# Optimization experiments

Hardware: AMD Instinct MI355X
Metric: run time of the kernel (lower is better)

Reference implementation:

```python
import jax, jax.numpy as jnp
import numpy as np
from itertools import combinations

SEQ_LEN = 8
FEAT = 2048
SET_SIZE = 2
DOUT = 1152
WAY = 5
SHOT = 5
NQ = 500
MAX_LEN = int(SEQ_LEN * 1.5)
LN_EPS = 1e-5

TUPLES = np.array(list(combinations(range(SEQ_LEN), SET_SIZE)), dtype=np.int32)  # [T, SET_SIZE]
T_LEN = TUPLES.shape[0]  # C(8,2) = 28

def _positional_encoding(d_model, max_len):
    pos = np.arange(max_len, dtype=np.float32)[:, None]
    div = np.exp(np.arange(0, d_model, 2, dtype=np.float32) * (-np.log(10000.0) / d_model))
    pe = np.zeros((max_len, d_model), dtype=np.float32)
    pe[:, 0::2] = np.sin(pos * div)
    pe[:, 1::2] = np.cos(pos * div)
    return jnp.asarray(pe)

PE = _positional_encoding(FEAT, MAX_LEN)  # dropout is identity in eval mode

def _layernorm(x, gamma, beta):
    mu = jnp.mean(x, axis=-1, keepdims=True)
    var = jnp.var(x, axis=-1, keepdims=True)
    return (x - mu) * jax.lax.rsqrt(var + LN_EPS) * gamma + beta

def setup_inputs() -> dict:
    key = jax.random.key(0)
    ks = jax.random.split(key, 8)
    din = FEAT * SET_SIZE
    sc = 1.0 / np.sqrt(din)
    return {
        "support_set": jax.random.normal(ks[0], (WAY * SHOT, SEQ_LEN, FEAT), jnp.float32),
        "support_labels": jnp.repeat(jnp.arange(WAY, dtype=jnp.int32), SHOT),  # sorted, balanced episode
        "queries": jax.random.normal(ks[1], (NQ, SEQ_LEN, FEAT), jnp.float32),
        "k_w": jax.random.normal(ks[2], (din, DOUT), jnp.float32) * sc,
        "k_b": jnp.zeros((DOUT,), jnp.float32),
        "v_w": jax.random.normal(ks[3], (din, DOUT), jnp.float32) * sc,
        "v_b": jnp.zeros((DOUT,), jnp.float32),
        "ln_k_gamma": jnp.ones((DOUT,), jnp.float32),
        "ln_k_beta": jnp.zeros((DOUT,), jnp.float32),
        "global_temperature": jnp.asarray(1.0, jnp.float32),
        "temperature_weight": jnp.ones((1,), jnp.float32),
    }

def reference(support_set, support_labels, queries, k_w, k_b, v_w, v_b,
              ln_k_gamma, ln_k_beta, global_temperature, temperature_weight):
    n_q = queries.shape[0]
    # positional encoding (dropout is eval-mode identity)
    s = support_set + PE[:SEQ_LEN]
    q = queries + PE[:SEQ_LEN]
    # gather frame tuples: [n, T, SET_SIZE, FEAT] -> [n, T, SET_SIZE*FEAT]
    s_t = s[:, TUPLES, :].reshape(WAY * SHOT, T_LEN, SET_SIZE * FEAT)
    q_t = q[:, TUPLES, :].reshape(n_q, T_LEN, SET_SIZE * FEAT)
    # K / V projections; LayerNorm only on K (as in the module)
    s_ks = _layernorm(s_t @ k_w + k_b, ln_k_gamma, ln_k_beta)
    q_ks = _layernorm(q_t @ k_w + k_b, ln_k_gamma, ln_k_beta)
    s_vs = s_t @ v_w + v_b
    q_vs = q_t @ v_w + v_b
    # labels are sorted & balanced -> per-class slices are a reshape
    class_k = s_ks.reshape(WAY, SHOT, T_LEN, DOUT)
    class_v = s_vs.reshape(WAY, SHOT, T_LEN, DOUT)
    # scores[c,q,t,k,u] = <q_ks[q,t], class_k[c,k,u]> / sqrt(DOUT)
    scores = jnp.einsum('qtd,ckud->cqtku', q_ks, class_k) / np.sqrt(DOUT)
    # softmax jointly over (support-clip k, support-tuple u) per query tuple t
    attn = jax.nn.softmax(scores.reshape(WAY, n_q, T_LEN, SHOT * T_LEN), axis=-1)
    attn = attn.reshape(WAY, n_q, T_LEN, SHOT, T_LEN)
    # prototype = sum over support clips of attn @ class_v
    proto = jnp.einsum('cqtku,ckud->cqtd', attn, class_v)  # [WAY, NQ, T, DOUT]
    diff = q_vs[None] - proto
    dist = jnp.sum(diff * diff, axis=(-2, -1)) / T_LEN  # [WAY, NQ]
    logits = (-dist * global_temperature * temperature_weight[0]).T  # [NQ, WAY]
    return logits
```

## Files before the change

### kernel.cpp

```cpp
#include <hip/hip_runtime.h>

typedef __bf16 bf16;
typedef __attribute__((ext_vector_type(8))) __bf16 bf16x8;
typedef __attribute__((ext_vector_type(4))) float f32x4;

#define AS1 __attribute__((address_space(1)))
#define AS3 __attribute__((address_space(3)))

__device__ __constant__ int c_T0[28] = {0,0,0,0,0,0,0,1,1,1,1,1,1,2,2,2,2,2,3,3,3,3,4,4,4,5,5,6};
__device__ __constant__ int c_T1[28] = {1,2,3,4,5,6,7,2,3,4,5,6,7,3,4,5,6,7,4,5,6,7,5,6,7,6,7,7};

__global__ __launch_bounds__(256) void fill_pack(
    const float* __restrict__ queries, const float* __restrict__ support,
    const float* __restrict__ kw, const float* __restrict__ vw,
    bf16* __restrict__ X, bf16* __restrict__ Wp)
{
    __shared__ float t[32][33];
    const int tid = threadIdx.x;
    if (blockIdx.x < 4224) {
        const int f = blockIdx.x;
        bf16* row = X + (long)f * 2048;
        const int d0 = tid << 3;
        if (f >= 4200) {
            bf16x8 z;
            #pragma unroll
            for (int i = 0; i < 8; ++i) z[i] = (bf16)0.f;
            *(bf16x8*)(row + d0) = z;
            return;
        }
        const float* src = (f < 4000) ? (queries + (long)f * 2048)
                                      : (support + (long)(f - 4000) * 2048);
        const int s = f & 7;
        bf16x8 o;
        #pragma unroll
        for (int i = 0; i < 8; ++i) {
            int d = d0 + i;
            float dv = __expf((float)(d >> 1) * -0.008994473019508f);
            float ang = (float)s * dv;
            float pe = (d & 1) ? __cosf(ang) : __sinf(ang);
            o[i] = (bf16)(src[d] + pe);
        }
        *(bf16x8*)(row + d0) = o;
    } else {
        const int b = blockIdx.x - 4224;
        const int k0 = (b & 63) << 5, n0g = (b >> 6) << 5;
        const int tx = tid & 31, ty = tid >> 5;
        const int j = n0g / 1152, nc = n0g % 1152;
        const float* src = ((j < 2) ? kw : vw) + (long)(((j & 1) << 11) + k0) * 1152 + nc;
        #pragma unroll
        for (int i = 0; i < 4; ++i)
            t[ty + (i << 3)][tx] = src[(long)(ty + (i << 3)) * 1152 + tx];
        __syncthreads();
        #pragma unroll
        for (int i = 0; i < 4; ++i)
            Wp[(long)(n0g + ty + (i << 3)) * 2048 + k0 + tx] = (bf16)t[tx][ty + (i << 3)];
    }
}

template <typename OutT>
__global__ __launch_bounds__(256) void gemm_bt(
    const bf16* __restrict__ A, long lda, const bf16* __restrict__ B, long ldb,
    OutT* __restrict__ C, int N, int K, float scale, int tiles_n)
{
    __shared__ __align__(16) bf16 lA[128 * 32];
    __shared__ __align__(16) bf16 lB[128 * 32];
    const int tid = threadIdx.x;
    const int wid = tid >> 6, lane = tid & 63;
    const int wm = (wid >> 1) << 6, wn = (wid & 1) << 6;
    const int quad = lane >> 4, l16 = lane & 15;
    const int tm = blockIdx.x / tiles_n, tn = blockIdx.x % tiles_n;
    const int m0 = tm << 7, n0 = tn << 7;
    const bf16* Abase = A + (long)m0 * lda;

    f32x4 acc[4][4];
    #pragma unroll
    for (int i = 0; i < 4; ++i)
        #pragma unroll
        for (int j = 0; j < 4; ++j)
            #pragma unroll
            for (int r = 0; r < 4; ++r) acc[i][j][r] = 0.f;

    const int srow = lane >> 2, scol = (lane & 3) << 3;
    for (int kk = 0; kk < K; kk += 32) {
        __syncthreads();
        #pragma unroll
        for (int p = 0; p < 2; ++p) {
            const int rbase = (wid << 5) + (p << 4);
            const bf16* ga = Abase + (long)(rbase + srow) * lda + kk + scol;
            const bf16* gb = B + (long)(n0 + rbase + srow) * ldb + kk + scol;
            __builtin_amdgcn_global_load_lds((const AS1 unsigned int*)ga,
                                             (AS3 unsigned int*)(lA + rbase * 32), 16, 0, 0);
            __builtin_amdgcn_global_load_lds((const AS1 unsigned int*)gb,
                                             (AS3 unsigned int*)(lB + rbase * 32), 16, 0, 0);
        }
        __builtin_amdgcn_s_waitcnt(0);
        __syncthreads();
        bf16x8 af[4], bfr[4];
        #pragma unroll
        for (int i = 0; i < 4; ++i)
            af[i] = *(const bf16x8*)(lA + (wm + (i << 4) + l16) * 32 + (quad << 3));
        #pragma unroll
        for (int j = 0; j < 4; ++j)
            bfr[j] = *(const bf16x8*)(lB + (wn + (j << 4) + l16) * 32 + (quad << 3));
        #pragma unroll
        for (int i = 0; i < 4; ++i)
            #pragma unroll
            for (int j = 0; j < 4; ++j)
                acc[i][j] = __builtin_amdgcn_mfma_f32_16x16x32_bf16(af[i], bfr[j], acc[i][j], 0, 0, 0);
    }
    #pragma unroll
    for (int i = 0; i < 4; ++i) {
        const int row = m0 + wm + (i << 4) + (quad << 2);
        #pragma unroll
        for (int j = 0; j < 4; ++j) {
            const int col = n0 + wn + (j << 4) + l16;
            OutT* cp = C + (long)row * N + col;
            #pragma unroll
            for (int r = 0; r < 4; ++r) cp[(long)r * N] = (OutT)(acc[i][j][r] * scale);
        }
    }
}

__global__ __launch_bounds__(256) void gemm_frames(
    const bf16* __restrict__ H, const bf16* __restrict__ Bk,
    const bf16* __restrict__ svs, bf16* __restrict__ FG, bf16* __restrict__ Gb)
{
    __shared__ __align__(16) bf16 lA[128 * 32];
    __shared__ __align__(16) bf16 lB[128 * 32];
    const int tid = threadIdx.x;
    const int wid = tid >> 6, lane = tid & 63;
    const int wm = (wid >> 1) << 6, wn = (wid & 1) << 6;
    const int quad = lane >> 4, l16 = lane & 15;
    const bool gram = (int)blockIdx.x >= 792;
    int seg = 4, tm, tn;
    const bf16* Abase;
    long la;
    const bf16* B;
    if (!gram) {
        seg = blockIdx.x / 198;
        int r = blockIdx.x % 198;
        tm = r / 6; tn = r % 6;
        Abase = H + seg * 1152 + (long)(tm << 7) * 4608;
        la = 4608;
        B = (seg < 2) ? Bk : svs;
    } else {
        int r = blockIdx.x - 792;
        tm = r / 6; tn = r % 6;
        Abase = svs + (long)(tm << 7) * 1152;
        la = 1152;
        B = svs;
    }
    const int n0 = tn << 7;

    f32x4 acc[4][4];
    #pragma unroll
    for (int i = 0; i < 4; ++i)
        #pragma unroll
        for (int j = 0; j < 4; ++j)
            #pragma unroll
            for (int r = 0; r < 4; ++r) acc[i][j][r] = 0.f;

    const int srow = lane >> 2, scol = (lane & 3) << 3;
    for (int kk = 0; kk < 1152; kk += 32) {
        __syncthreads();
        #pragma unroll
        for (int p = 0; p < 2; ++p) {
            const int rbase = (wid << 5) + (p << 4);
            const bf16* ga = Abase + (long)(rbase + srow) * la + kk + scol;
            const bf16* gb = B + (long)(n0 + rbase + srow) * 1152 + kk + scol;
            __builtin_amdgcn_global_load_lds((const AS1 unsigned int*)ga,
                                             (AS3 unsigned int*)(lA + rbase * 32), 16, 0, 0);
            __builtin_amdgcn_global_load_lds((const AS1 unsigned int*)gb,
                                             (AS3 unsigned int*)(lB + rbase * 32), 16, 0, 0);
        }
        __builtin_amdgcn_s_waitcnt(0);
        __syncthreads();
        bf16x8 af[4], bfr[4];
        #pragma unroll
        for (int i = 0; i < 4; ++i)
            af[i] = *(const bf16x8*)(lA + (wm + (i << 4) + l16) * 32 + (quad << 3));
        #pragma unroll
        for (int j = 0; j < 4; ++j)
            bfr[j] = *(const bf16x8*)(lB + (wn + (j << 4) + l16) * 32 + (quad << 3));
        #pragma unroll
        for (int i = 0; i < 4; ++i)
            #pragma unroll
            for (int j = 0; j < 4; ++j)
                acc[i][j] = __builtin_amdgcn_mfma_f32_16x16x32_bf16(af[i], bfr[j], acc[i][j], 0, 0, 0);
    }
    #pragma unroll
    for (int i = 0; i < 4; ++i) {
        const int rloc = (tm << 7) + wm + (i << 4) + (quad << 2);
        #pragma unroll
        for (int j = 0; j < 4; ++j) {
            const int col = n0 + wn + (j << 4) + l16;
            #pragma unroll
            for (int r = 0; r < 4; ++r) {
                const int row = rloc + r;
                if (!gram) {
                    FG[(long)(seg * 4224 + row) * 768 + col] = (bf16)acc[i][j][r];
                } else {
                    bool keep = (row < 700) && (col < 700) && (row / 140 == col / 140);
                    Gb[(long)row * 768 + col] = keep ? (bf16)acc[i][j][r] : (bf16)0.f;
                }
            }
        }
    }
}

__global__ __launch_bounds__(256) void support_stats(
    const bf16* __restrict__ H, const float* __restrict__ kb,
    const float* __restrict__ vb, const float* __restrict__ gamma,
    const float* __restrict__ beta,
    bf16* __restrict__ Bk, bf16* __restrict__ svs,
    float* __restrict__ gd, float* __restrict__ kbd,
    float* __restrict__ bd2, float* __restrict__ bdot,
    float* __restrict__ MU, float* __restrict__ RS, float* __restrict__ QS)
{
    __shared__ __align__(16) char smem[2 * 9216 * 2 + 512];
    const int tid = threadIdx.x;
    const int wid = tid >> 6, lane = tid & 63;
    if ((int)blockIdx.x < 768) {
        const int u = blockIdx.x;
        bf16* outK = Bk + (long)u * 1152;
        bf16* outV = svs + (long)u * 1152;
        if (u >= 700) {
            for (int d = tid; d < 1152; d += 256) { outK[d] = (bf16)0.f; outV[d] = (bf16)0.f; }
            if (tid == 0) { gd[u] = 0.f; kbd[u] = 0.f; bd2[u] = 0.f; bdot[u] = 0.f; }
            return;
        }
        float* s1 = (float*)smem;
        float* s2 = s1 + 4;
        float* sr = s2 + 4;
        const int n = u / 28, t = u - n * 28;
        const int fi = 4000 + (n << 3) + c_T0[t];
        const int fj = 4000 + (n << 3) + c_T1[t];
        const bf16* Hi = H + (long)fi * 4608;
        const bf16* Hj = H + (long)fj * 4608;
        float xv[5];
        float sum = 0.f, sumsq = 0.f;
        #pragma unroll
        for (int it = 0; it < 5; ++it) {
            int d = tid + (it << 8);
            float x = 0.f;
            if (d < 1152) {
                x = (float)Hi[d] + (float)Hj[1152 + d] + kb[d];
                sum += x; sumsq += x * x;
            }
            xv[it] = x;
        }
        #pragma unroll
        for (int off = 32; off > 0; off >>= 1) {
            sum += __shfl_xor(sum, off, 64);
            sumsq += __shfl_xor(sumsq, off, 64);
        }
        if ((tid & 63) == 0) { s1[wid] = sum; s2[wid] = sumsq; }
        __syncthreads();
        sum = s1[0] + s1[1] + s1[2] + s1[3];
        sumsq = s2[0] + s2[1] + s2[2] + s2[3];
        const float mu = sum * (1.f / 1152.f);
        const float var = sumsq * (1.f / 1152.f) - mu * mu;
        const float rs = rsqrtf(var + 1e-5f);
        float g_ = 0.f, k_ = 0.f, b_ = 0.f, v_ = 0.f;
        #pragma unroll
        for (int it = 0; it < 5; ++it) {
            int d = tid + (it << 8);
            if (d < 1152) {
                float gm = gamma[d];
                float sk = (xv[it] - mu) * rs * gm + beta[d];
                outK[d] = (bf16)(gm * sk);
                g_ += gm * sk;
                k_ += kb[d] * gm * sk;
                b_ += beta[d] * sk;
                float sv = (float)Hi[2304 + d] + (float)Hj[3456 + d] + vb[d];
                outV[d] = (bf16)sv;
                v_ += vb[d] * sv;
            }
        }
        #pragma unroll
        for (int off = 32; off > 0; off >>= 1) {
            g_ += __shfl_xor(g_, off, 64);
            k_ += __shfl_xor(k_, off, 64);
            b_ += __shfl_xor(b_, off, 64);
            v_ += __shfl_xor(v_, off, 64);
        }
        if ((tid & 63) == 0) { sr[wid * 4 + 0] = g_; sr[wid * 4 + 1] = k_; sr[wid * 4 + 2] = b_; sr[wid * 4 + 3] = v_; }
        __syncthreads();
        if (tid == 0) {
            gd[u]   = sr[0] + sr[4] + sr[8]  + sr[12];
            kbd[u]  = sr[1] + sr[5] + sr[9]  + sr[13];
            bd2[u]  = sr[2] + sr[6] + sr[10] + sr[14];
            bdot[u] = sr[3] + sr[7] + sr[11] + sr[15];
        }
        return;
    }
    const int s_ = blockIdx.x - 768;
    const bool kside = s_ < 500;
    const int q = kside ? s_ : s_ - 500;
    const int co = kside ? 0 : 2304;
    const float* bias = kside ? kb : vb;
    bf16* Ft = (bf16*)smem;
    bf16* Fb = Ft + 9216;
    float* fl = (float*)(smem + 36864);
    float* Sa = fl;
    float* Qa = fl + 8;
    float* Ca = fl + 16;
    float* Sb_ = fl + 24;
    float* Qb_ = fl + 32;
    float* Cb_ = fl + 40;
    float* Pp = fl + 48;
    float* Sk2 = fl + 76;
    for (int idx = tid; idx < 1152; idx += 256) {
        int row = idx / 144, col = (idx - row * 144) << 3;
        const bf16* src = H + (long)((q << 3) + row) * 4608 + co;
        *(bf16x8*)(Ft + row * 1152 + col) = *(const bf16x8*)(src + col);
        *(bf16x8*)(Fb + row * 1152 + col) = *(const bf16x8*)(src + 1152 + col);
    }
    __syncthreads();
    for (int task = wid; task < 45; task += 4) {
        float s0 = 0.f, s1v = 0.f, s2v = 0.f;
        if (task < 16) {
            const bf16* p = (task < 8) ? (Ft + task * 1152) : (Fb + (task - 8) * 1152);
            for (int c = lane << 3; c < 1152; c += 512) {
                bf16x8 v = *(const bf16x8*)(p + c);
                #pragma unroll
                for (int k = 0; k < 8; ++k) {
                    float f = (float)v[k];
                    s0 += f; s1v += f * f; s2v += f * bias[c + k];
                }
            }
        } else if (task < 44) {
            int t = task - 16;
            const bf16* pa = Ft + c_T0[t] * 1152;
            const bf16* pb = Fb + c_T1[t] * 1152;
            for (int c = lane << 3; c < 1152; c += 512) {
                bf16x8 a = *(const bf16x8*)(pa + c);
                bf16x8 b = *(const bf16x8*)(pb + c);
                #pragma unroll
                for (int k = 0; k < 8; ++k) s0 += (float)a[k] * (float)b[k];
            }
        } else {
            for (int c = lane << 3; c < 1152; c += 512) {
                #pragma unroll
                for (int k = 0; k < 8; ++k) { float f = bias[c + k]; s0 += f; s1v += f * f; }
            }
        }
        #pragma unroll
        for (int off = 32; off > 0; off >>= 1) {
            s0 += __shfl_xor(s0, off, 64);
            s1v += __shfl_xor(s1v, off, 64);
            s2v += __shfl_xor(s2v, off, 64);
        }
        if (lane == 0) {
            if (task < 8)       { Sa[task] = s0; Qa[task] = s1v; Ca[task] = s2v; }
            else if (task < 16) { Sb_[task - 8] = s0; Qb_[task - 8] = s1v; Cb_[task - 8] = s2v; }
            else if (task < 44) Pp[task - 16] = s0;
            else                { Sk2[0] = s0; Sk2[1] = s1v; }
        }
    }
    __syncthreads();
    if (kside) {
        if (tid < 28) {
            int i = c_T0[tid], j = c_T1[tid];
            float mu = (Sa[i] + Sb_[j] + Sk2[0]) * (1.f / 1152.f);
            float ex2 = (Qa[i] + Qb_[j] + Sk2[1] + 2.f * (Pp[tid] + Ca[i] + Cb_[j])) * (1.f / 1152.f);
            float var = ex2 - mu * mu;
            int m = q * 28 + tid;
            MU[m] = mu;
            RS[m] = rsqrtf(var + 1e-5f);
        }
    } else {
        if (tid < 64) {
            float term = 0.f;
            if (lane < 28) {
                int i = c_T0[lane], j = c_T1[lane];
                term = Qa[i] + Qb_[j] + Sk2[1] + 2.f * (Pp[lane] + Ca[i] + Cb_[j]);
            }
            #pragma unroll
            for (int off = 32; off > 0; off >>= 1) term += __shfl_xor(term, off, 64);
            if (lane == 0) QS[q] = term;
        }
    }
}

__global__ __launch_bounds__(320) void assemble_softmax(
    const bf16* __restrict__ Fkt, const bf16* __restrict__ Fkb,
    const float* __restrict__ MU, const float* __restrict__ RS,
    const float* __restrict__ gd, const float* __restrict__ kbd,
    const float* __restrict__ bd2, bf16* __restrict__ attn)
{
    const int m = blockIdx.x, tid = threadIdx.x;
    bf16* arow = attn + (long)m * 768;
    if (m >= 14000) {
        for (int d = tid; d < 768; d += 320) arow[d] = (bf16)0.f;
        return;
    }
    if (tid < 68) arow[700 + tid] = (bf16)0.f;
    const int q = m / 28, t = m - q * 28;
    const bf16* ft = Fkt + (long)((q << 3) + c_T0[t]) * 768;
    const bf16* fb = Fkb + (long)((q << 3) + c_T1[t]) * 768;
    const float mu = MU[m], rs = RS[m];
    const int w = tid >> 6, lane = tid & 63;
    const int base = w * 140;
    const float sc = 0.029462782549439484f;
    int u0 = base + lane, u1 = base + 64 + lane, u2 = base + 128 + lane;
    float v0 = (rs * ((float)ft[u0] + (float)fb[u0] + kbd[u0] - mu * gd[u0]) + bd2[u0]) * sc;
    float v1 = (rs * ((float)ft[u1] + (float)fb[u1] + kbd[u1] - mu * gd[u1]) + bd2[u1]) * sc;
    float v2 = (lane < 12)
             ? (rs * ((float)ft[u2] + (float)fb[u2] + kbd[u2] - mu * gd[u2]) + bd2[u2]) * sc
             : -1e30f;
    float mx = fmaxf(fmaxf(v0, v1), v2);
    #pragma unroll
    for (int off = 32; off > 0; off >>= 1) mx = fmaxf(mx, __shfl_xor(mx, off, 64));
    float e0 = __expf(v0 - mx), e1 = __expf(v1 - mx);
    float e2 = (lane < 12) ? __expf(v2 - mx) : 0.f;
    float s = e0 + e1 + e2;
    #pragma unroll
    for (int off = 32; off > 0; off >>= 1) s += __shfl_xor(s, off, 64);
    const float inv = 1.f / s;
    bf16* aw = arow + base;
    aw[lane] = (bf16)(e0 * inv);
    aw[64 + lane] = (bf16)(e1 * inv);
    if (lane < 12) aw[128 + lane] = (bf16)(e2 * inv);
}

__global__ __launch_bounds__(256) void final_dist(
    const bf16* __restrict__ attn, const bf16* __restrict__ attnG,
    const bf16* __restrict__ FG, const float* __restrict__ bdot,
    float* __restrict__ dist)
{
    const int w = threadIdx.x >> 6, lane = threadIdx.x & 63;
    const int m = blockIdx.x * 4 + w;
    const int q = m / 28, t = m - q * 28;
    const int fi = (q << 3) + c_T0[t], fj = (q << 3) + c_T1[t];
    const bf16* ar = attn + (long)m * 768;
    const bf16* gr = attnG + (long)m * 768;
    const bf16* ft = FG + (long)(8448 + fi) * 768;
    const bf16* fb = FG + (long)(12672 + fj) * 768;
    #pragma unroll
    for (int c = 0; c < 5; ++c) {
        const int base = c * 140;
        float s = 0.f;
        {
            int u = base + lane;
            float wv = (float)ft[u] + (float)fb[u] + bdot[u];
            s += (float)ar[u] * ((float)gr[u] - 2.f * wv);
        }
        {
            int u = base + 64 + lane;
            float wv = (float)ft[u] + (float)fb[u] + bdot[u];
            s += (float)ar[u] * ((float)gr[u] - 2.f * wv);
        }
        if (lane < 12) {
            int u = base + 128 + lane;
            float wv = (float)ft[u] + (float)fb[u] + bdot[u];
            s += (float)ar[u] * ((float)gr[u] - 2.f * wv);
        }
        #pragma unroll
        for (int off = 32; off > 0; off >>= 1) s += __shfl_xor(s, off, 64);
        if (lane == 0) atomicAdd(&dist[c * 500 + q], s);
    }
}

__global__ void finalize(const float* __restrict__ dist, const float* __restrict__ QS,
                         const float* __restrict__ gt, const float* __restrict__ tw,
                         float* __restrict__ out)
{
    int i = blockIdx.x * 256 + threadIdx.x;
    if (i < 2500) {
        int q = i / 5, c = i - q * 5;
        out[i] = -(dist[c * 500 + q] + QS[q]) * (gt[0] * tw[0] * (1.f / 28.f));
    }
}

extern "C" void kernel_launch(void* const* d_in, const int* in_sizes, int n_in,
                              void* d_out, int out_size, void* d_ws, size_t ws_size,
                              hipStream_t stream)
{
    const float* support = (const float*)d_in[0];
    const float* queries = (const float*)d_in[2];
    const float* kw      = (const float*)d_in[3];
    const float* kb      = (const float*)d_in[4];
    const float* vw      = (const float*)d_in[5];
    const float* vb      = (const float*)d_in[6];
    const float* gamma   = (const float*)d_in[7];
    const float* beta    = (const float*)d_in[8];
    const float* gt      = (const float*)d_in[9];
    const float* tw      = (const float*)d_in[10];
    float* out = (float*)d_out;

    char* ws = (char*)d_ws;
    size_t off = 0;
    auto alloc = [&](size_t b) { char* p = ws + off; off += (b + 255) & ~(size_t)255; return p; };
    bf16* X      = (bf16*)alloc(4224ull * 2048 * 2);
    bf16* Wp     = (bf16*)alloc(4608ull * 2048 * 2);
    char* uni    = alloc(14080ull * 768 * 4);
    bf16* H      = (bf16*)uni;
    bf16* attn   = (bf16*)uni;
    bf16* attnG  = (bf16*)(uni + 14080ull * 768 * 2);
    bf16* FG     = (bf16*)alloc(16896ull * 768 * 2);
    bf16* Bk     = (bf16*)alloc(768ull * 1152 * 2);
    bf16* svs    = (bf16*)alloc(768ull * 1152 * 2);
    bf16* Gb     = (bf16*)alloc(768ull * 768 * 2);
    float* MU    = (float*)alloc(14000ull * 4);
    float* RS    = (float*)alloc(14000ull * 4);
    float* gd    = (float*)alloc(768 * 4);
    float* kbd   = (float*)alloc(768 * 4);
    float* bd2   = (float*)alloc(768 * 4);
    float* bdot  = (float*)alloc(768 * 4);
    float* QS    = (float*)alloc(500 * 4);
    float* dist  = (float*)alloc(5 * 500 * 4);

    hipMemsetAsync(dist, 0, 5 * 500 * 4, stream);
    fill_pack<<<4224 + 9216, 256, 0, stream>>>(queries, support, kw, vw, X, Wp);
    gemm_bt<bf16><<<33 * 36, 256, 0, stream>>>(X, 2048, Wp, 2048, H, 4608, 2048, 1.f, 36);
    support_stats<<<1768, 256, 0, stream>>>(H, kb, vb, gamma, beta, Bk, svs,
                                            gd, kbd, bd2, bdot, MU, RS, QS);
    gemm_frames<<<828, 256, 0, stream>>>(H, Bk, svs, FG, Gb);
    assemble_softmax<<<14080, 320, 0, stream>>>(FG, FG + 4224ull * 768, MU, RS, gd, kbd, bd2, attn);
    gemm_bt<bf16><<<110 * 6, 256, 0, stream>>>(attn, 768, Gb, 768, attnG, 768, 768, 1.f, 6);
    final_dist<<<3500, 256, 0, stream>>>(attn, attnG, FG + 0, bdot, dist);
    finalize<<<10, 256, 0, stream>>>(dist, QS, gt, tw, out);
}
```

Before: 419.2 us.

## Exploit block-diagonal Gram: per-class attn layout and fused class GEMM with distance

Attention is stored per class in a [5][14080][144] layout and the support Gram matrix as five 140x140 diagonal blocks, replacing the dense 768x768 block-diagonal GEMM that mostly multiplied zeros. A new class_dist kernel loads each class's attention tile and Gram block into LDS, does the small MFMA product, and fuses the distance reduction, so the attnG buffer and the separate final_dist pass are no longer needed. H no longer aliases the attention buffers, which costs extra workspace. The single memset now covers both G5 and dist, relying on the two allocations being adjacent.

```diff
diff --git a/kernel.cpp b/kernel.cpp
--- a/kernel.cpp
+++ b/kernel.cpp
@@ -123,7 +123,7 @@
 
 __global__ __launch_bounds__(256) void gemm_frames(
     const bf16* __restrict__ H, const bf16* __restrict__ Bk,
-    const bf16* __restrict__ svs, bf16* __restrict__ FG, bf16* __restrict__ Gb)
+    const bf16* __restrict__ svs, bf16* __restrict__ FG, bf16* __restrict__ G5)
 {
     __shared__ __align__(16) bf16 lA[128 * 32];
     __shared__ __align__(16) bf16 lB[128 * 32];
@@ -200,8 +200,11 @@
                 if (!gram) {
                     FG[(long)(seg * 4224 + row) * 768 + col] = (bf16)acc[i][j][r];
                 } else {
-                    bool keep = (row < 700) && (col < 700) && (row / 140 == col / 140);
-                    Gb[(long)row * 768 + col] = keep ? (bf16)acc[i][j][r] : (bf16)0.f;
+                    if (row < 700 && col < 700 && row / 140 == col / 140) {
+                        int cc = row / 140;
+                        G5[((long)cc * 144 + (row - cc * 140)) * 160 + (col - cc * 140)]
+                            = (bf16)acc[i][j][r];
+                    }
                 }
             }
         }
@@ -387,15 +390,16 @@
     const bf16* __restrict__ Fkt, const bf16* __restrict__ Fkb,
     const float* __restrict__ MU, const float* __restrict__ RS,
     const float* __restrict__ gd, const float* __restrict__ kbd,
-    const float* __restrict__ bd2, bf16* __restrict__ attn)
+    const float* __restrict__ bd2, bf16* __restrict__ attn5)
 {
     const int m = blockIdx.x, tid = threadIdx.x;
-    bf16* arow = attn + (long)m * 768;
     if (m >= 14000) {
-        for (int d = tid; d < 768; d += 320) arow[d] = (bf16)0.f;
+        #pragma unroll
+        for (int c = 0; c < 5; ++c)
+            for (int d = tid; d < 144; d += 320)
+                attn5[((long)c * 14080 + m) * 144 + d] = (bf16)0.f;
         return;
     }
-    if (tid < 68) arow[700 + tid] = (bf16)0.f;
     const int q = m / 28, t = m - q * 28;
     const bf16* ft = Fkt + (long)((q << 3) + c_T0[t]) * 768;
     const bf16* fb = Fkb + (long)((q << 3) + c_T1[t]) * 768;
@@ -418,47 +422,86 @@
     #pragma unroll
     for (int off = 32; off > 0; off >>= 1) s += __shfl_xor(s, off, 64);
     const float inv = 1.f / s;
-    bf16* aw = arow + base;
+    bf16* aw = attn5 + ((long)w * 14080 + m) * 144;
     aw[lane] = (bf16)(e0 * inv);
     aw[64 + lane] = (bf16)(e1 * inv);
     if (lane < 12) aw[128 + lane] = (bf16)(e2 * inv);
-}
-
-__global__ __launch_bounds__(256) void final_dist(
-    const bf16* __restrict__ attn, const bf16* __restrict__ attnG,
+    else if (lane < 16) aw[128 + lane] = (bf16)0.f;
+}
+
+__global__ __launch_bounds__(256) void class_dist(
+    const bf16* __restrict__ attn5, const bf16* __restrict__ G5,
     const bf16* __restrict__ FG, const float* __restrict__ bdot,
     float* __restrict__ dist)
 {
-    const int w = threadIdx.x >> 6, lane = threadIdx.x & 63;
-    const int m = blockIdx.x * 4 + w;
-    const int q = m / 28, t = m - q * 28;
-    const int fi = (q << 3) + c_T0[t], fj = (q << 3) + c_T1[t];
-    const bf16* ar = attn + (long)m * 768;
-    const bf16* gr = attnG + (long)m * 768;
-    const bf16* ft = FG + (long)(8448 + fi) * 768;
-    const bf16* fb = FG + (long)(12672 + fj) * 768;
-    #pragma unroll
-    for (int c = 0; c < 5; ++c) {
-        const int base = c * 140;
-        float s = 0.f;
-        {
-            int u = base + lane;
-            float wv = (float)ft[u] + (float)fb[u] + bdot[u];
-            s += (float)ar[u] * ((float)gr[u] - 2.f * wv);
-        }
-        {
-            int u = base + 64 + lane;
-            float wv = (float)ft[u] + (float)fb[u] + bdot[u];
-            s += (float)ar[u] * ((float)gr[u] - 2.f * wv);
-        }
-        if (lane < 12) {
-            int u = base + 128 + lane;
-            float wv = (float)ft[u] + (float)fb[u] + bdot[u];
-            s += (float)ar[u] * ((float)gr[u] - 2.f * wv);
-        }
-        #pragma unroll
-        for (int off = 32; off > 0; off >>= 1) s += __shfl_xor(s, off, 64);
-        if (lane == 0) atomicAdd(&dist[c * 500 + q], s);
+    __shared__ __align__(16) bf16 lA[128 * 168];
+    __shared__ __align__(16) bf16 lG[144 * 168];
+    const int tid = threadIdx.x;
+    const int c = blockIdx.x / 110, tm = blockIdx.x % 110;
+    const long m0 = (long)tm * 128;
+    const bf16* Abase = attn5 + ((long)c * 14080 + m0) * 144;
+    for (int v = tid; v < 128 * 18; v += 256) {
+        int r = v / 18, k = (v - r * 18) << 3;
+        *(bf16x8*)(lA + r * 168 + k) = *(const bf16x8*)(Abase + (long)r * 144 + k);
+    }
+    {
+        int r = tid >> 1, k = 144 + ((tid & 1) << 3);
+        bf16x8 z;
+        #pragma unroll
+        for (int i = 0; i < 8; ++i) z[i] = (bf16)0.f;
+        *(bf16x8*)(lA + r * 168 + k) = z;
+    }
+    const bf16* Gbase = G5 + (long)c * 144 * 160;
+    for (int v = tid; v < 144 * 20; v += 256) {
+        int r = v / 20, k = (v - r * 20) << 3;
+        *(bf16x8*)(lG + r * 168 + k) = *(const bf16x8*)(Gbase + r * 160 + k);
+    }
+    __syncthreads();
+    const int wid = tid >> 6, lane = tid & 63;
+    const int quad = lane >> 4, l16 = lane & 15;
+    const int wr = wid << 5;
+    f32x4 acc[2][9];
+    #pragma unroll
+    for (int i = 0; i < 2; ++i)
+        #pragma unroll
+        for (int j = 0; j < 9; ++j)
+            #pragma unroll
+            for (int r = 0; r < 4; ++r) acc[i][j][r] = 0.f;
+    #pragma unroll
+    for (int kk = 0; kk < 160; kk += 32) {
+        bf16x8 af0 = *(const bf16x8*)(lA + (wr + l16) * 168 + kk + (quad << 3));
+        bf16x8 af1 = *(const bf16x8*)(lA + (wr + 16 + l16) * 168 + kk + (quad << 3));
+        #pragma unroll
+        for (int j = 0; j < 9; ++j) {
+            bf16x8 bf_ = *(const bf16x8*)(lG + ((j << 4) + l16) * 168 + kk + (quad << 3));
+            acc[0][j] = __builtin_amdgcn_mfma_f32_16x16x32_bf16(af0, bf_, acc[0][j], 0, 0, 0);
+            acc[1][j] = __builtin_amdgcn_mfma_f32_16x16x32_bf16(af1, bf_, acc[1][j], 0, 0, 0);
+        }
+    }
+    #pragma unroll
+    for (int i = 0; i < 2; ++i) {
+        #pragma unroll
+        for (int r = 0; r < 4; ++r) {
+            const int rl = wr + (i << 4) + (quad << 2) + r;
+            const long m = m0 + rl;
+            if (m >= 14000) continue;
+            const int q = (int)(m / 28), t = (int)(m - (long)q * 28);
+            const int fi = (q << 3) + c_T0[t], fj = (q << 3) + c_T1[t];
+            const bf16* ft = FG + (long)(8448 + fi) * 768 + c * 140;
+            const bf16* fb = FG + (long)(12672 + fj) * 768 + c * 140;
+            const float* bd = bdot + c * 140;
+            float s = 0.f;
+            #pragma unroll
+            for (int j = 0; j < 9; ++j) {
+                const int col = (j << 4) + l16;
+                float a = (float)lA[rl * 168 + col];
+                float wv = (float)ft[col] + (float)fb[col] + bd[col];
+                s += a * (acc[i][j][r] - 2.f * wv);
+            }
+            #pragma unroll
+            for (int off = 1; off < 16; off <<= 1) s += __shfl_xor(s, off, 64);
+            if (l16 == 0) atomicAdd(&dist[c * 500 + q], s);
+        }
     }
 }
 
@@ -494,14 +537,13 @@
     auto alloc = [&](size_t b) { char* p = ws + off; off += (b + 255) & ~(size_t)255; return p; };
     bf16* X      = (bf16*)alloc(4224ull * 2048 * 2);
     bf16* Wp     = (bf16*)alloc(4608ull * 2048 * 2);
-    char* uni    = alloc(14080ull * 768 * 4);
-    bf16* H      = (bf16*)uni;
-    bf16* attn   = (bf16*)uni;
-    bf16* attnG  = (bf16*)(uni + 14080ull * 768 * 2);
+    bf16* H      = (bf16*)alloc(4224ull * 4608 * 2);
     bf16* FG     = (bf16*)alloc(16896ull * 768 * 2);
+    bf16* attn5  = (bf16*)alloc(5ull * 14080 * 144 * 2);
     bf16* Bk     = (bf16*)alloc(768ull * 1152 * 2);
     bf16* svs    = (bf16*)alloc(768ull * 1152 * 2);
-    bf16* Gb     = (bf16*)alloc(768ull * 768 * 2);
+    bf16* G5     = (bf16*)alloc(5ull * 144 * 160 * 2);
+    float* dist  = (float*)alloc(5 * 500 * 4);
     float* MU    = (float*)alloc(14000ull * 4);
     float* RS    = (float*)alloc(14000ull * 4);
     float* gd    = (float*)alloc(768 * 4);
@@ -509,16 +551,14 @@
     float* bd2   = (float*)alloc(768 * 4);
     float* bdot  = (float*)alloc(768 * 4);
     float* QS    = (float*)alloc(500 * 4);
-    float* dist  = (float*)alloc(5 * 500 * 4);
-
-    hipMemsetAsync(dist, 0, 5 * 500 * 4, stream);
+
+    hipMemsetAsync(G5, 0, 5ull * 144 * 160 * 2 + 5 * 500 * 4, stream);
     fill_pack<<<4224 + 9216, 256, 0, stream>>>(queries, support, kw, vw, X, Wp);
     gemm_bt<bf16><<<33 * 36, 256, 0, stream>>>(X, 2048, Wp, 2048, H, 4608, 2048, 1.f, 36);
     support_stats<<<1768, 256, 0, stream>>>(H, kb, vb, gamma, beta, Bk, svs,
                                             gd, kbd, bd2, bdot, MU, RS, QS);
-    gemm_frames<<<828, 256, 0, stream>>>(H, Bk, svs, FG, Gb);
-    assemble_softmax<<<14080, 320, 0, stream>>>(FG, FG + 4224ull * 768, MU, RS, gd, kbd, bd2, attn);
-    gemm_bt<bf16><<<110 * 6, 256, 0, stream>>>(attn, 768, Gb, 768, attnG, 768, 768, 1.f, 6);
-    final_dist<<<3500, 256, 0, stream>>>(attn, attnG, FG + 0, bdot, dist);
+    gemm_frames<<<828, 256, 0, stream>>>(H, Bk, svs, FG, G5);
+    assemble_softmax<<<14080, 320, 0, stream>>>(FG, FG + 4224ull * 768, MU, RS, gd, kbd, bd2, attn5);
+    class_dist<<<550, 256, 0, stream>>>(attn5, G5, FG, bdot, dist);
     finalize<<<10, 256, 0, stream>>>(dist, QS, gt, tw, out);
 }
```

Measured after the change: 399.9 us. 4.6% less time.
